# Performance work log

Hardware: AMD Instinct MI355X
Metric: run time of the kernel (lower is better)

Reference implementation:

```python
import jax, jax.numpy as jnp
import numpy as np
import math

N, E, D, H = 1536, 49152, 512, 8
DH = D // H  # head dim = 64
SCALE = 256.0 * math.sqrt(2.0)  # rel_dists scaling in forward


def sinusoidal_pe(x, d):
    """x: [...] float positions -> [..., d] interleaved sin/cos encoding."""
    div = jnp.exp(jnp.arange(0, d, 2, dtype=jnp.float32) * (-math.log(10000.0) / d))
    ang = x[..., None] * div  # [..., d//2]
    return jnp.stack([jnp.sin(ang), jnp.cos(ang)], axis=-1).reshape(*x.shape, d)


def setup_inputs() -> dict:
    key = jax.random.key(0)
    ks = jax.random.split(key, 8)
    features = jax.random.normal(ks[0], (N, D), dtype=jnp.float32)
    edge_index = jax.random.randint(ks[1], (2, E), 0, N, dtype=jnp.int64)
    edge_attr = jax.random.uniform(ks[2], (E,), dtype=jnp.float32)  # normalized distances
    pos = jax.random.uniform(ks[3], (N, 2), dtype=jnp.float32)  # unused by forward
    s = 1.0 / math.sqrt(D)  # ~xavier-uniform bound sqrt(6/(D+D))... use simple symmetric init
    Wq = jax.random.uniform(ks[4], (D, D), minval=-s, maxval=s, dtype=jnp.float32)
    Wk = jax.random.uniform(ks[5], (D, D), minval=-s, maxval=s, dtype=jnp.float32)
    Wv = jax.random.uniform(ks[6], (D, D), minval=-s, maxval=s, dtype=jnp.float32)
    bq = jnp.zeros((D,), jnp.float32)
    bk = jnp.zeros((D,), jnp.float32)
    bv = jnp.zeros((D,), jnp.float32)
    return dict(features=features, edge_index=edge_index, edge_attr=edge_attr, pos=pos,
                Wq=Wq, bq=bq, Wk=Wk, bk=bk, Wv=Wv, bv=bv)


def reference(features, edge_index, edge_attr, pos, Wq, bq, Wk, bk, Wv, bv):
    # batch dim is 1 in the original (features.unsqueeze(0)); we omit it.
    q = (features @ Wq.T + bq).reshape(N, H, DH).transpose(1, 0, 2)  # [H,N,DH]
    k = (features @ Wk.T + bk).reshape(N, H, DH).transpose(1, 0, 2)
    v = (features @ Wv.T + bv).reshape(N, H, DH).transpose(1, 0, 2)

    qk = jnp.einsum('hqd,hrd->hqr', q, k)  # [H,N,N]

    # to_dense_adj: scatter-add edge_attr into dense [N,N], then scale
    rel = jnp.zeros((N, N), jnp.float32).at[edge_index[0], edge_index[1]].add(edge_attr) * SCALE
    # embed_k and embed_q are identical parameter-free sinusoidal encodings of rel
    rk = sinusoidal_pe(rel, DH)  # [N,N,DH]

    # original: qk + q.rk + k.rq + (q_repeat*k_repeat == qk)  => 2*qk + q.rk + k.rk
    logits = 2.0 * qk \
        + jnp.einsum('hqd,qrd->hqr', q, rk) \
        + jnp.einsum('hrd,qrd->hqr', k, rk)
    attn = jax.nn.softmax(logits / math.sqrt(DH), axis=-1)  # [H,N,N]

    out = jnp.einsum('hqr,hrd->hqd', attn, v)  # [H,N,DH]
    out = out.transpose(1, 0, 2).reshape(N, D)  # [N,D]
    return out.max(axis=0)  # [D] max-pool over nodes (MIL pooling)
```

## Files before the change

### kernel.cpp

```cpp
#include <hip/hip_runtime.h>
#include <cmath>


constexpr int Nn  = 1536;
constexpr int Dd  = 512;
constexpr int Hh  = 8;
constexpr int DHd = 64;
constexpr int SPLITS = 6;
constexpr float SCALE_F = 362.03867196751236f;
constexpr float M0 = 8.0f;

typedef float f4 __attribute__((ext_vector_type(4)));
typedef int   i4 __attribute__((ext_vector_type(4)));
typedef __attribute__((ext_vector_type(4))) float f32x4;
typedef __attribute__((ext_vector_type(8))) short bf16x8;

__device__ inline unsigned short bf16_rne(float x) {
    unsigned u = __float_as_uint(x);
    unsigned r = u + 0x7fff + ((u >> 16) & 1);
    return (unsigned short)(r >> 16);
}
__device__ inline float bf16_tof(unsigned short h) {
    return __uint_as_float(((unsigned)h) << 16);
}
__device__ inline unsigned f2ord(float x) {
    unsigned b = __float_as_uint(x);
    return (b & 0x80000000u) ? ~b : (b | 0x80000000u);
}

__global__ __launch_bounds__(256) void pack_fw_k(
    const float* __restrict__ feat,
    const float* __restrict__ Wq, const float* __restrict__ Wk, const float* __restrict__ Wv,
    unsigned short* __restrict__ pFh, unsigned short* __restrict__ pFl,
    unsigned short* __restrict__ pWh, unsigned short* __restrict__ pWl)
{
    int tg = blockIdx.x * 256 + threadIdx.x;
    int type = blockIdx.y;
    int L = tg & 63;
    int kc = (tg >> 6) & 15;
    int t10 = tg >> 10;
    const float* src;
    unsigned short *oh, *ol;
    int row, col;
    if (type == 0) {
        src = feat; oh = pFh; ol = pFl;
        row = t10 * 16 + (L & 15);
        col = kc * 32 + (L >> 4) * 8;
    } else {
        int z = t10 >> 5, nt = t10 & 31;
        src = (z == 0) ? Wq : (z == 1) ? Wk : Wv;
        oh = pWh; ol = pWl;
        row = nt * 16 + (L & 15);
        col = kc * 32 + (L >> 4) * 8;
    }
    f4 a = *(const f4*)(src + (size_t)row * Dd + col);
    f4 b = *(const f4*)(src + (size_t)row * Dd + col + 4);
    float x[8];
    #pragma unroll
    for (int j = 0; j < 4; ++j) { x[j] = a[j]; x[4 + j] = b[j]; }
    unsigned short hs[8], ls[8];
    #pragma unroll
    for (int j = 0; j < 8; ++j) {
        hs[j] = bf16_rne(x[j]);
        ls[j] = bf16_rne(x[j] - bf16_tof(hs[j]));
    }
    *(bf16x8*)(oh + (size_t)tg * 8) = *(bf16x8*)hs;
    *(bf16x8*)(ol + (size_t)tg * 8) = *(bf16x8*)ls;
}

__global__ __launch_bounds__(256) void qkvm_k(
    const unsigned short* __restrict__ pFh, const unsigned short* __restrict__ pFl,
    const unsigned short* __restrict__ pWh, const unsigned short* __restrict__ pWl,
    const float* __restrict__ bq, const float* __restrict__ bk, const float* __restrict__ bv,
    float* __restrict__ Qo, float* __restrict__ Ko, float* __restrict__ Vo)
{
    const int z = blockIdx.z;
    const float* __restrict__ bias = (z == 0) ? bq : (z == 1) ? bk : bv;
    float* __restrict__ outp       = (z == 0) ? Qo : (z == 1) ? Ko : Vo;
    const int tid = threadIdx.x;
    const int L = tid & 63, wv = tid >> 6;
    const int l15 = L & 15, quad = L >> 4;
    const int mt0 = blockIdx.y * 4 + (wv & 1) * 2;
    const int nt0 = blockIdx.x * 4 + (wv >> 1) * 2;

    f32x4 acc[2][2];
    #pragma unroll
    for (int i = 0; i < 2; ++i)
        #pragma unroll
        for (int j = 0; j < 2; ++j) acc[i][j] = (f32x4){0.f, 0.f, 0.f, 0.f};

    bf16x8 AH[2][2], AL[2][2], BH[2][2], BL[2][2];
    auto loadset = [&](int buf, int kc) {
        #pragma unroll
        for (int i = 0; i < 2; ++i) {
            size_t ao = ((size_t)((mt0 + i) * 16 + kc)) * 512 + L * 8;
            AH[buf][i] = *(const bf16x8*)(pFh + ao);
            AL[buf][i] = *(const bf16x8*)(pFl + ao);
            size_t bo = ((size_t)((z * 32 + nt0 + i) * 16 + kc)) * 512 + L * 8;
            BH[buf][i] = *(const bf16x8*)(pWh + bo);
            BL[buf][i] = *(const bf16x8*)(pWl + bo);
        }
    };
    auto mfmaset = [&](int buf) {
        #pragma unroll
        for (int i = 0; i < 2; ++i)
            #pragma unroll
            for (int j = 0; j < 2; ++j) {
                f32x4 a = acc[i][j];
                a = __builtin_amdgcn_mfma_f32_16x16x32_bf16(AH[buf][i], BH[buf][j], a, 0, 0, 0);
                a = __builtin_amdgcn_mfma_f32_16x16x32_bf16(AH[buf][i], BL[buf][j], a, 0, 0, 0);
                a = __builtin_amdgcn_mfma_f32_16x16x32_bf16(AL[buf][i], BH[buf][j], a, 0, 0, 0);
                a = __builtin_amdgcn_mfma_f32_16x16x32_bf16(AL[buf][i], BL[buf][j], a, 0, 0, 0);
                acc[i][j] = a;
            }
    };

    loadset(0, 0);
    #pragma unroll
    for (int kc = 0; kc < 16; kc += 2) {
        loadset(1, kc + 1);
        mfmaset(0);
        if (kc + 2 < 16) loadset(0, kc + 2);
        mfmaset(1);
    }

    #pragma unroll
    for (int i = 0; i < 2; ++i) {
        int row0 = (mt0 + i) * 16 + quad * 4;
        #pragma unroll
        for (int j = 0; j < 2; ++j) {
            int col = (nt0 + j) * 16 + l15;
            float b = bias[col];
            #pragma unroll
            for (int reg = 0; reg < 4; ++reg)
                outp[(size_t)(row0 + reg) * Dd + col] = acc[i][j][reg] + b;
        }
    }
}

__global__ __launch_bounds__(256) void pack_k(
    const float* __restrict__ Q, const float* __restrict__ K, const float* __restrict__ V,
    unsigned short* __restrict__ pQh, unsigned short* __restrict__ pQl,
    unsigned short* __restrict__ pKh, unsigned short* __restrict__ pKl,
    unsigned short* __restrict__ pVh, unsigned short* __restrict__ pVl)
{
    int tg = blockIdx.x * 256 + threadIdx.x;
    int type = blockIdx.y;
    int L = tg & 63;
    float x[8];
    unsigned short* oh;
    unsigned short* ol;
    if (type < 2) {
        const float* src = type ? K : Q;
        oh = type ? pKh : pQh;
        ol = type ? pKl : pQl;
        int kc = (tg >> 6) & 1;
        int mt = (tg >> 7) % 96;
        int h  = (tg >> 7) / 96;
        int row = mt * 16 + (L & 15);
        int col = h * 64 + kc * 32 + (L >> 4) * 8;
        f4 a = *(const f4*)(src + (size_t)row * Dd + col);
        f4 b = *(const f4*)(src + (size_t)row * Dd + col + 4);
        float sc = type ? 1.0f : 0.25f;
        #pragma unroll
        for (int j = 0; j < 4; ++j) { x[j] = a[j] * sc; x[4 + j] = b[j] * sc; }
    } else {
        oh = pVh; ol = pVl;
        int dt = (tg >> 6) & 3;
        int rc = (tg >> 8) % 48;
        int h  = (tg >> 8) / 48;
        int col  = h * 64 + dt * 16 + (L & 15);
        int row0 = rc * 32 + (L >> 4) * 8;
        #pragma unroll
        for (int j = 0; j < 8; ++j) x[j] = V[(size_t)(row0 + j) * Dd + col];
    }
    unsigned short hs[8], ls[8];
    #pragma unroll
    for (int j = 0; j < 8; ++j) {
        hs[j] = bf16_rne(x[j]);
        ls[j] = bf16_rne(x[j] - bf16_tof(hs[j]));
    }
    *(bf16x8*)(oh + (size_t)tg * 8) = *(bf16x8*)hs;
    *(bf16x8*)(ol + (size_t)tg * 8) = *(bf16x8*)ls;
}

__global__ __launch_bounds__(256) void init_rel_k(float* __restrict__ rel,
                                                  int* __restrict__ eid,
                                                  unsigned* __restrict__ ordmax)
{
    size_t idx = (size_t)blockIdx.x * 256 + threadIdx.x;
    size_t i = idx * 4;
    if (i < (size_t)Nn * Nn) {
        *(f4*)(rel + i) = (f4){0.f, 0.f, 0.f, 0.f};
        *(i4*)(eid + i) = (i4){-1, -1, -1, -1};
    }
    if (idx < 128) {
        #pragma unroll
        for (int c = 0; c < 4; ++c) ordmax[idx * 4 + c] = 0x007FFFFFu;
    }
}

__global__ __launch_bounds__(256) void scatter_k(
    const int* __restrict__ raw, const float* __restrict__ attr,
    float* __restrict__ rel, int* __restrict__ eid, int* __restrict__ idxn, int E)
{
    int e = blockIdx.x * 256 + threadIdx.x;
    if (e >= E) return;
    int acc = 0;
    #pragma unroll
    for (int i = 0; i < 16; ++i) acc |= raw[2 * i + 1];
    int s, t;
    if (acc == 0) { s = raw[2 * e]; t = raw[2 * (E + e)]; }
    else          { s = raw[e];     t = raw[E + e]; }
    idxn[e] = s; idxn[E + e] = t;
    size_t off = (size_t)s * Nn + t;
    atomicAdd(rel + off, attr[e] * SCALE_F);
    eid[off] = e;
}

__global__ void oddsum_k(const float* __restrict__ Q, const float* __restrict__ K,
                         float* __restrict__ qodd, float* __restrict__ kodd,
                         float* __restrict__ koddT)
{
    int t = blockIdx.x * 256 + threadIdx.x;
    if (t >= 2 * Nn * Hh) return;
    const float* src = (t < Nn * Hh) ? Q : K;
    int i = (t < Nn * Hh) ? t : t - Nn * Hh;
    int n = i >> 3, h = i & 7;
    const float* row = src + (size_t)n * Dd + h * DHd;
    float s = 0.f;
    #pragma unroll
    for (int ii = 0; ii < 32; ++ii) s += row[2 * ii + 1];
    if (t < Nn * Hh) qodd[i] = s;
    else { kodd[i] = s; koddT[h * Nn + n] = 0.125f * s; }
}

__global__ __launch_bounds__(256) void delta_k(
    const int* __restrict__ idxn, const float* __restrict__ rel,
    const float* __restrict__ Q, const float* __restrict__ K,
    const float* __restrict__ qodd, const float* __restrict__ kodd,
    float* __restrict__ delta8, int E)
{
    int t = blockIdx.x * 256 + threadIdx.x;
    if (t >= E * Hh) return;
    int e = t >> 3, h = t & 7;
    int qi = idxn[e], ri = idxn[E + e];
    float x = rel[(size_t)qi * Nn + ri];
    const float* qrow = Q + (size_t)qi * Dd + h * DHd;
    const float* krow = K + (size_t)ri * Dd + h * DHd;
    float acc = 0.f;
    #pragma unroll
    for (int i = 0; i < 32; i += 2) {
        float dd0 = 0.15915494309189535f * __builtin_amdgcn_exp2f(-0.4152410118609203f * (float)i);
        float dd1 = 0.15915494309189535f * __builtin_amdgcn_exp2f(-0.4152410118609203f * (float)(i + 1));
        float r0 = x * dd0; r0 -= floorf(r0);
        float r1 = x * dd1; r1 -= floorf(r1);
        float s0 = __builtin_amdgcn_sinf(r0), c0 = __builtin_amdgcn_cosf(r0);
        float s1 = __builtin_amdgcn_sinf(r1), c1 = __builtin_amdgcn_cosf(r1);
        f4 q4 = *(const f4*)(qrow + 2 * i);
        f4 k4 = *(const f4*)(krow + 2 * i);
        acc += (q4[0] + k4[0]) * s0 + (q4[1] + k4[1]) * c0
             + (q4[2] + k4[2]) * s1 + (q4[3] + k4[3]) * c1;
    }
    delta8[(size_t)e * Hh + h] = 0.125f * (acc - qodd[qi * Hh + h] - kodd[ri * Hh + h]);
}

__global__ __launch_bounds__(64, 4) void flash6_k(
    const unsigned short* __restrict__ pQh, const unsigned short* __restrict__ pQl,
    const unsigned short* __restrict__ pKh, const unsigned short* __restrict__ pKl,
    const unsigned short* __restrict__ pVh, const unsigned short* __restrict__ pVl,
    const int* __restrict__ eid, const float* __restrict__ delta8,
    const float* __restrict__ koddT,
    float* __restrict__ Opart, float* __restrict__ Lpart)
{
    const int qt = blockIdx.x, h = blockIdx.y, s = blockIdx.z;
    const int L = threadIdx.x, quad = L >> 4, l15 = L & 15;
    const int q0 = qt * 16;
    __shared__ unsigned short phi[16][80];
    __shared__ unsigned short plo[16][80];

    bf16x8 qh[2], ql[2];
    #pragma unroll
    for (int kc = 0; kc < 2; ++kc) {
        size_t off = ((size_t)((h * 96 + qt) * 2 + kc)) * 512 + L * 8;
        qh[kc] = *(const bf16x8*)(pQh + off);
        ql[kc] = *(const bf16x8*)(pQl + off);
    }

    f32x4 O[4];
    float lsum[4];
    #pragma unroll
    for (int r = 0; r < 4; ++r) { lsum[r] = 0.f; O[r] = (f32x4){0.f, 0.f, 0.f, 0.f}; }

    const int NT = 24 / SPLITS;
    const int Tbase = s * NT;

    bf16x8 kh0[4], kh1[4], kl0[4], kl1[4];
    {
        const int r0 = Tbase * 64;
        #pragma unroll
        for (int nt = 0; nt < 4; ++nt) {
            size_t b0 = ((size_t)((h * 96 + (r0 >> 4) + nt) * 2)) * 512 + L * 8;
            kh0[nt] = *(const bf16x8*)(pKh + b0);
            kh1[nt] = *(const bf16x8*)(pKh + b0 + 512);
            kl0[nt] = *(const bf16x8*)(pKl + b0);
            kl1[nt] = *(const bf16x8*)(pKl + b0 + 512);
        }
    }

    float kvcur[4], dcur[16];
    {
        const int r0 = Tbase * 64;
        int ecur[16];
        #pragma unroll
        for (int nt = 0; nt < 4; ++nt) {
            kvcur[nt] = koddT[h * Nn + r0 + nt * 16 + l15];
            #pragma unroll
            for (int reg = 0; reg < 4; ++reg)
                ecur[nt * 4 + reg] = eid[(size_t)(q0 + quad * 4 + reg) * Nn + r0 + nt * 16 + l15];
        }
        #pragma unroll
        for (int i = 0; i < 16; ++i) {
            int e = ecur[i];
            float d = delta8[(size_t)(e < 0 ? 0 : e) * Hh + h];
            dcur[i] = (e >= 0) ? d : 0.f;
        }
    }

    for (int T = 0; T < NT; ++T) {
        const int r0 = (Tbase + T) * 64;
        const bool more = (T + 1 < NT);

        int   enxt[16];
        float kvnxt[4];
        if (more) {
            const int r1 = r0 + 64;
            #pragma unroll
            for (int nt = 0; nt < 4; ++nt) {
                kvnxt[nt] = koddT[h * Nn + r1 + nt * 16 + l15];
                #pragma unroll
                for (int reg = 0; reg < 4; ++reg)
                    enxt[nt * 4 + reg] = eid[(size_t)(q0 + quad * 4 + reg) * Nn + r1 + nt * 16 + l15];
            }
        }

        bf16x8 vh0[4], vh1[4], vl0[4], vl1[4];
        #pragma unroll
        for (int dt = 0; dt < 4; ++dt) {
            size_t vb = ((size_t)((h * 48 + (r0 >> 5)) * 4 + dt)) * 512 + L * 8;
            vh0[dt] = *(const bf16x8*)(pVh + vb);
            vh1[dt] = *(const bf16x8*)(pVh + vb + 2048);
            vl0[dt] = *(const bf16x8*)(pVl + vb);
            vl1[dt] = *(const bf16x8*)(pVl + vb + 2048);
        }

        f32x4 S[4];
        #pragma unroll
        for (int nt = 0; nt < 4; ++nt) {
            f32x4 a = {0.f, 0.f, 0.f, 0.f};
            a = __builtin_amdgcn_mfma_f32_16x16x32_bf16(qh[0], kh0[nt], a, 0, 0, 0);
            a = __builtin_amdgcn_mfma_f32_16x16x32_bf16(qh[1], kh1[nt], a, 0, 0, 0);
            a = __builtin_amdgcn_mfma_f32_16x16x32_bf16(qh[0], kl0[nt], a, 0, 0, 0);
            a = __builtin_amdgcn_mfma_f32_16x16x32_bf16(qh[1], kl1[nt], a, 0, 0, 0);
            a = __builtin_amdgcn_mfma_f32_16x16x32_bf16(ql[0], kh0[nt], a, 0, 0, 0);
            a = __builtin_amdgcn_mfma_f32_16x16x32_bf16(ql[1], kh1[nt], a, 0, 0, 0);
            S[nt] = a;
        }

        if (more) {
            const int r1 = r0 + 64;
            #pragma unroll
            for (int nt = 0; nt < 4; ++nt) {
                size_t b0 = ((size_t)((h * 96 + (r1 >> 4) + nt) * 2)) * 512 + L * 8;
                kh0[nt] = *(const bf16x8*)(pKh + b0);
                kh1[nt] = *(const bf16x8*)(pKh + b0 + 512);
                kl0[nt] = *(const bf16x8*)(pKl + b0);
                kl1[nt] = *(const bf16x8*)(pKl + b0 + 512);
            }
        }

        #pragma unroll
        for (int reg = 0; reg < 4; ++reg) {
            float p[4];
            #pragma unroll
            for (int nt = 0; nt < 4; ++nt) {
                p[nt] = __expf(S[nt][reg] + kvcur[nt] + dcur[nt * 4 + reg] - M0);
                lsum[reg] += p[nt];
                unsigned short hi = bf16_rne(p[nt]);
                phi[quad * 4 + reg][nt * 16 + l15] = hi;
                plo[quad * 4 + reg][nt * 16 + l15] = bf16_rne(p[nt] - bf16_tof(hi));
            }
        }

        bf16x8 ph[2], pl[2];
        #pragma unroll
        for (int kc2 = 0; kc2 < 2; ++kc2) {
            ph[kc2] = *(const bf16x8*)&phi[l15][kc2 * 32 + quad * 8];
            pl[kc2] = *(const bf16x8*)&plo[l15][kc2 * 32 + quad * 8];
        }

        #pragma unroll
        for (int dt = 0; dt < 4; ++dt) {
            f32x4 a = O[dt];
            a = __builtin_amdgcn_mfma_f32_16x16x32_bf16(ph[0], vh0[dt], a, 0, 0, 0);
            a = __builtin_amdgcn_mfma_f32_16x16x32_bf16(ph[1], vh1[dt], a, 0, 0, 0);
            a = __builtin_amdgcn_mfma_f32_16x16x32_bf16(ph[0], vl0[dt], a, 0, 0, 0);
            a = __builtin_amdgcn_mfma_f32_16x16x32_bf16(ph[1], vl1[dt], a, 0, 0, 0);
            a = __builtin_amdgcn_mfma_f32_16x16x32_bf16(pl[0], vh0[dt], a, 0, 0, 0);
            a = __builtin_amdgcn_mfma_f32_16x16x32_bf16(pl[1], vh1[dt], a, 0, 0, 0);
            O[dt] = a;
        }

        if (more) {
            #pragma unroll
            for (int i = 0; i < 16; ++i) {
                int e = enxt[i];
                float d = delta8[(size_t)(e < 0 ? 0 : e) * Hh + h];
                dcur[i] = (e >= 0) ? d : 0.f;
            }
            #pragma unroll
            for (int nt = 0; nt < 4; ++nt) kvcur[nt] = kvnxt[nt];
        }
    }

    #pragma unroll
    for (int reg = 0; reg < 4; ++reg) {
        #pragma unroll
        for (int o = 1; o < 16; o <<= 1) lsum[reg] += __shfl_xor(lsum[reg], o);
    }

    #pragma unroll
    for (int dt = 0; dt < 4; ++dt)
        #pragma unroll
        for (int reg = 0; reg < 4; ++reg)
            Opart[((size_t)(s * Hh + h) * Nn + q0 + quad * 4 + reg) * 64 + dt * 16 + l15] = O[dt][reg];
    if (l15 == 0) {
        #pragma unroll
        for (int reg = 0; reg < 4; ++reg)
            Lpart[(size_t)(s * Hh + h) * Nn + q0 + quad * 4 + reg] = lsum[reg];
    }
}

__global__ __launch_bounds__(256) void combine_mp_k(
    const float* __restrict__ Opart, const float* __restrict__ Lpart,
    unsigned* __restrict__ ordmax)
{
    const int b = blockIdx.x;
    const int t = threadIdx.x;
    const int cg = (t & 127) * 4;
    const int h = cg >> 6, d = cg & 63;
    const int rh = t >> 7;
    f4 mx = {-3.0e38f, -3.0e38f, -3.0e38f, -3.0e38f};
    for (int r = 0; r < 8; ++r) {
        int q = b * 16 + rh * 8 + r;
        float l = 0.f;
        f4 o = {0.f, 0.f, 0.f, 0.f};
        #pragma unroll
        for (int s2 = 0; s2 < SPLITS; ++s2) {
            l += Lpart[(size_t)(s2 * Hh + h) * Nn + q];
            f4 ov = *(const f4*)(Opart + ((size_t)(s2 * Hh + h) * Nn + q) * 64 + d);
            #pragma unroll
            for (int c = 0; c < 4; ++c) o[c] += ov[c];
        }
        float inv = 1.0f / l;
        #pragma unroll
        for (int c = 0; c < 4; ++c) mx[c] = fmaxf(mx[c], o[c] * inv);
    }
    #pragma unroll
    for (int c = 0; c < 4; ++c) atomicMax(&ordmax[cg + c], f2ord(mx[c]));
}

__global__ void decode_k(const unsigned* __restrict__ ordmax, float* __restrict__ outp)
{
    int t = blockIdx.x * 256 + threadIdx.x;
    if (t >= Dd) return;
    unsigned u = ordmax[t];
    outp[t] = (u & 0x80000000u) ? __uint_as_float(u ^ 0x80000000u) : __uint_as_float(~u);
}

extern "C" void kernel_launch(void* const* d_in, const int* in_sizes, int n_in,
                              void* d_out, int out_size, void* d_ws, size_t ws_size,
                              hipStream_t stream)
{
    const float* feat   = (const float*)d_in[0];
    const int*   rawidx = (const int*)d_in[1];
    const float* attr   = (const float*)d_in[2];
    const float* Wq = (const float*)d_in[4];
    const float* bq = (const float*)d_in[5];
    const float* Wk = (const float*)d_in[6];
    const float* bk = (const float*)d_in[7];
    const float* Wv = (const float*)d_in[8];
    const float* bv = (const float*)d_in[9];
    float* outp = (float*)d_out;
    const int E = in_sizes[2];

    const size_t ND_ = (size_t)Nn * Dd;
    const size_t NN_ = (size_t)Nn * Nn;
    const size_t PK_ = (size_t)Hh * 96 * 2 * 512;
    float* ws    = (float*)d_ws;
    float* Q     = ws;
    float* K     = Q + ND_;
    float* V     = K + ND_;
    unsigned short* pFh = (unsigned short*)(V + ND_);
    unsigned short* pFl = pFh + PK_;
    unsigned short* pWh = pFl + PK_;
    unsigned short* pWl = pWh + PK_;
    float* rel   = (float*)(pWl + PK_);
    int*   eid   = (int*)(rel + NN_);
    float* delta8 = (float*)(eid + NN_);
    float* qodd  = delta8 + (size_t)E * Hh;
    float* kodd  = qodd + (size_t)Nn * Hh;
    float* koddT = kodd + (size_t)Nn * Hh;
    int*   idxn  = (int*)(koddT + (size_t)Nn * Hh);
    unsigned short* pQh = (unsigned short*)(idxn + 2 * E);
    unsigned short* pQl = pQh + PK_;
    unsigned short* pKh = pQl + PK_;
    unsigned short* pKl = pKh + PK_;
    unsigned short* pVh = pKl + PK_;
    unsigned short* pVl = pVh + PK_;
    float* Lpart = (float*)(pVl + PK_);
    unsigned* ordmax = (unsigned*)(Lpart + (size_t)SPLITS * Hh * Nn);
    float* Opart = ws;

    pack_fw_k<<<dim3(384, 2), 256, 0, stream>>>(feat, Wq, Wk, Wv, pFh, pFl, pWh, pWl);
    qkvm_k<<<dim3(8, 24, 3), 256, 0, stream>>>(pFh, pFl, pWh, pWl, bq, bk, bv, Q, K, V);
    init_rel_k<<<(int)((NN_ / 4 + 255) / 256), 256, 0, stream>>>(rel, eid, ordmax);
    scatter_k<<<(E + 255) / 256, 256, 0, stream>>>(rawidx, attr, rel, eid, idxn, E);
    oddsum_k<<<(2 * Nn * Hh + 255) / 256, 256, 0, stream>>>(Q, K, qodd, kodd, koddT);
    delta_k<<<(E * Hh + 255) / 256, 256, 0, stream>>>(idxn, rel, Q, K, qodd, kodd, delta8, E);
    pack_k<<<dim3(384, 3), 256, 0, stream>>>(Q, K, V, pQh, pQl, pKh, pKl, pVh, pVl);
    flash6_k<<<dim3(96, 8, SPLITS), 64, 0, stream>>>(pQh, pQl, pKh, pKl, pVh, pVl,
                                                     eid, delta8, koddT, Opart, Lpart);
    combine_mp_k<<<96, 256, 0, stream>>>(Opart, Lpart, ordmax);
    decode_k<<<(Dd + 255) / 256, 256, 0, stream>>>(ordmax, outp);
}
```

Baseline: 221.2 us.

## Fuse QKV bf16 hi/lo packing into projection GEMM epilogue and reduce flash splits

```diff
diff --git a/kernel.cpp b/kernel.cpp
--- a/kernel.cpp
+++ b/kernel.cpp
@@ -6,7 +6,7 @@
 constexpr int Dd  = 512;
 constexpr int Hh  = 8;
 constexpr int DHd = 64;
-constexpr int SPLITS = 6;
+constexpr int SPLITS = 4;
 constexpr float SCALE_F = 362.03867196751236f;
 constexpr float M0 = 8.0f;
 
@@ -72,16 +72,19 @@
     const unsigned short* __restrict__ pFh, const unsigned short* __restrict__ pFl,
     const unsigned short* __restrict__ pWh, const unsigned short* __restrict__ pWl,
     const float* __restrict__ bq, const float* __restrict__ bk, const float* __restrict__ bv,
-    float* __restrict__ Qo, float* __restrict__ Ko, float* __restrict__ Vo)
+    float* __restrict__ Qo, float* __restrict__ Ko,
+    unsigned short* __restrict__ pQh, unsigned short* __restrict__ pQl,
+    unsigned short* __restrict__ pKh, unsigned short* __restrict__ pKl,
+    unsigned short* __restrict__ pVh, unsigned short* __restrict__ pVl)
 {
     const int z = blockIdx.z;
     const float* __restrict__ bias = (z == 0) ? bq : (z == 1) ? bk : bv;
-    float* __restrict__ outp       = (z == 0) ? Qo : (z == 1) ? Ko : Vo;
     const int tid = threadIdx.x;
     const int L = tid & 63, wv = tid >> 6;
     const int l15 = L & 15, quad = L >> 4;
     const int mt0 = blockIdx.y * 4 + (wv & 1) * 2;
     const int nt0 = blockIdx.x * 4 + (wv >> 1) * 2;
+    __shared__ float lds[4][32][33];
 
     f32x4 acc[2][2];
     #pragma unroll
@@ -124,64 +127,77 @@
         mfmaset(1);
     }
 
-    #pragma unroll
-    for (int i = 0; i < 2; ++i) {
-        int row0 = (mt0 + i) * 16 + quad * 4;
+    float o_[2][2][4];
+    #pragma unroll
+    for (int i = 0; i < 2; ++i)
         #pragma unroll
         for (int j = 0; j < 2; ++j) {
-            int col = (nt0 + j) * 16 + l15;
-            float b = bias[col];
+            float b = bias[(nt0 + j) * 16 + l15];
+            #pragma unroll
+            for (int reg = 0; reg < 4; ++reg) o_[i][j][reg] = acc[i][j][reg] + b;
+        }
+    if (z < 2) {
+        float* __restrict__ outp = (z == 0) ? Qo : Ko;
+        #pragma unroll
+        for (int i = 0; i < 2; ++i) {
+            int row0 = (mt0 + i) * 16 + quad * 4;
+            #pragma unroll
+            for (int j = 0; j < 2; ++j) {
+                int col = (nt0 + j) * 16 + l15;
+                #pragma unroll
+                for (int reg = 0; reg < 4; ++reg)
+                    outp[(size_t)(row0 + reg) * Dd + col] = o_[i][j][reg];
+            }
+        }
+    }
+    #pragma unroll
+    for (int i = 0; i < 2; ++i)
+        #pragma unroll
+        for (int j = 0; j < 2; ++j)
             #pragma unroll
             for (int reg = 0; reg < 4; ++reg)
-                outp[(size_t)(row0 + reg) * Dd + col] = acc[i][j][reg] + b;
-        }
-    }
-}
-
-__global__ __launch_bounds__(256) void pack_k(
-    const float* __restrict__ Q, const float* __restrict__ K, const float* __restrict__ V,
-    unsigned short* __restrict__ pQh, unsigned short* __restrict__ pQl,
-    unsigned short* __restrict__ pKh, unsigned short* __restrict__ pKl,
-    unsigned short* __restrict__ pVh, unsigned short* __restrict__ pVl)
-{
-    int tg = blockIdx.x * 256 + threadIdx.x;
-    int type = blockIdx.y;
-    int L = tg & 63;
-    float x[8];
-    unsigned short* oh;
-    unsigned short* ol;
-    if (type < 2) {
-        const float* src = type ? K : Q;
-        oh = type ? pKh : pQh;
-        ol = type ? pKl : pQl;
-        int kc = (tg >> 6) & 1;
-        int mt = (tg >> 7) % 96;
-        int h  = (tg >> 7) / 96;
-        int row = mt * 16 + (L & 15);
-        int col = h * 64 + kc * 32 + (L >> 4) * 8;
-        f4 a = *(const f4*)(src + (size_t)row * Dd + col);
-        f4 b = *(const f4*)(src + (size_t)row * Dd + col + 4);
-        float sc = type ? 1.0f : 0.25f;
-        #pragma unroll
-        for (int j = 0; j < 4; ++j) { x[j] = a[j] * sc; x[4 + j] = b[j] * sc; }
+                lds[wv][i * 16 + quad * 4 + reg][j * 16 + l15] = o_[i][j][reg];
+
+    const int h = blockIdx.x;
+    if (z < 2) {
+        unsigned short* __restrict__ oh = z ? pKh : pQh;
+        unsigned short* __restrict__ ol = z ? pKl : pQl;
+        const int kc = wv >> 1;
+        const float sc = z ? 1.0f : 0.25f;
+        #pragma unroll
+        for (int i = 0; i < 2; ++i) {
+            float x[8]; unsigned short hs[8], ls[8];
+            #pragma unroll
+            for (int j2 = 0; j2 < 8; ++j2)
+                x[j2] = lds[wv][i * 16 + l15][quad * 8 + j2] * sc;
+            #pragma unroll
+            for (int j2 = 0; j2 < 8; ++j2) {
+                hs[j2] = bf16_rne(x[j2]);
+                ls[j2] = bf16_rne(x[j2] - bf16_tof(hs[j2]));
+            }
+            size_t off = ((size_t)((h * 96 + mt0 + i) * 2 + kc)) * 512 + L * 8;
+            *(bf16x8*)(oh + off) = *(bf16x8*)hs;
+            *(bf16x8*)(ol + off) = *(bf16x8*)ls;
+        }
     } else {
-        oh = pVh; ol = pVl;
-        int dt = (tg >> 6) & 3;
-        int rc = (tg >> 8) % 48;
-        int h  = (tg >> 8) / 48;
-        int col  = h * 64 + dt * 16 + (L & 15);
-        int row0 = rc * 32 + (L >> 4) * 8;
-        #pragma unroll
-        for (int j = 0; j < 8; ++j) x[j] = V[(size_t)(row0 + j) * Dd + col];
-    }
-    unsigned short hs[8], ls[8];
-    #pragma unroll
-    for (int j = 0; j < 8; ++j) {
-        hs[j] = bf16_rne(x[j]);
-        ls[j] = bf16_rne(x[j] - bf16_tof(hs[j]));
-    }
-    *(bf16x8*)(oh + (size_t)tg * 8) = *(bf16x8*)hs;
-    *(bf16x8*)(ol + (size_t)tg * 8) = *(bf16x8*)ls;
+        const int rc = blockIdx.y * 2 + (wv & 1);
+        #pragma unroll
+        for (int dtl = 0; dtl < 2; ++dtl) {
+            int dt = (wv >> 1) * 2 + dtl;
+            float x[8]; unsigned short hs[8], ls[8];
+            #pragma unroll
+            for (int j2 = 0; j2 < 8; ++j2)
+                x[j2] = lds[wv][quad * 8 + j2][dtl * 16 + l15];
+            #pragma unroll
+            for (int j2 = 0; j2 < 8; ++j2) {
+                hs[j2] = bf16_rne(x[j2]);
+                ls[j2] = bf16_rne(x[j2] - bf16_tof(hs[j2]));
+            }
+            size_t off = ((size_t)((h * 48 + rc) * 4 + dt)) * 512 + L * 8;
+            *(bf16x8*)(pVh + off) = *(bf16x8*)hs;
+            *(bf16x8*)(pVl + off) = *(bf16x8*)ls;
+        }
+    }
 }
 
 __global__ __launch_bounds__(256) void init_rel_k(float* __restrict__ rel,
@@ -265,7 +281,7 @@
     delta8[(size_t)e * Hh + h] = 0.125f * (acc - qodd[qi * Hh + h] - kodd[ri * Hh + h]);
 }
 
-__global__ __launch_bounds__(64, 4) void flash6_k(
+__global__ __launch_bounds__(64, 3) void flash5_k(
     const unsigned short* __restrict__ pQh, const unsigned short* __restrict__ pQl,
     const unsigned short* __restrict__ pKh, const unsigned short* __restrict__ pKl,
     const unsigned short* __restrict__ pVh, const unsigned short* __restrict__ pVl,
@@ -500,8 +516,7 @@
     float* ws    = (float*)d_ws;
     float* Q     = ws;
     float* K     = Q + ND_;
-    float* V     = K + ND_;
-    unsigned short* pFh = (unsigned short*)(V + ND_);
+    unsigned short* pFh = (unsigned short*)(K + ND_);
     unsigned short* pFl = pFh + PK_;
     unsigned short* pWh = pFl + PK_;
     unsigned short* pWl = pWh + PK_;
@@ -523,13 +538,13 @@
     float* Opart = ws;
 
     pack_fw_k<<<dim3(384, 2), 256, 0, stream>>>(feat, Wq, Wk, Wv, pFh, pFl, pWh, pWl);
-    qkvm_k<<<dim3(8, 24, 3), 256, 0, stream>>>(pFh, pFl, pWh, pWl, bq, bk, bv, Q, K, V);
+    qkvm_k<<<dim3(8, 24, 3), 256, 0, stream>>>(pFh, pFl, pWh, pWl, bq, bk, bv,
+                                               Q, K, pQh, pQl, pKh, pKl, pVh, pVl);
     init_rel_k<<<(int)((NN_ / 4 + 255) / 256), 256, 0, stream>>>(rel, eid, ordmax);
     scatter_k<<<(E + 255) / 256, 256, 0, stream>>>(rawidx, attr, rel, eid, idxn, E);
     oddsum_k<<<(2 * Nn * Hh + 255) / 256, 256, 0, stream>>>(Q, K, qodd, kodd, koddT);
     delta_k<<<(E * Hh + 255) / 256, 256, 0, stream>>>(idxn, rel, Q, K, qodd, kodd, delta8, E);
-    pack_k<<<dim3(384, 3), 256, 0, stream>>>(Q, K, V, pQh, pQl, pKh, pKl, pVh, pVl);
-    flash6_k<<<dim3(96, 8, SPLITS), 64, 0, stream>>>(pQh, pQl, pKh, pKl, pVh, pVl,
+    flash5_k<<<dim3(96, 8, SPLITS), 64, 0, stream>>>(pQh, pQl, pKh, pKl, pVh, pVl,
                                                      eid, delta8, koddT, Opart, Lpart);
     combine_mp_k<<<96, 256, 0, stream>>>(Opart, Lpart, ordmax);
     decode_k<<<(Dd + 255) / 256, 256, 0, stream>>>(ordmax, outp);
```

Result: faster. 196.7 us (-11.1%).
